# Kernel optimization log

Hardware: AMD Instinct MI355X
Metric: run time of the kernel (lower is better)

## Reference

```python
import jax, jax.numpy as jnp
import numpy as np

NPOINT = 2048
NSAMPLE = 16
LEAKY = 0.1
BN_EPS = 1e-5


def square_distance(src, dst):
    # src [B,S,3], dst [B,N,3] -> [B,S,N] squared euclidean
    d = -2.0 * jnp.einsum('bsc,bnc->bsn', src, dst)
    d = d + jnp.sum(src * src, -1)[:, :, None]
    d = d + jnp.sum(dst * dst, -1)[:, None, :]
    return d


def furthest_point_sample(xyz, npoint):
    # xyz [B,N,3] -> idx [B,npoint]; matches pointnet2 CUDA (seed = index 0)
    B, N, _ = xyz.shape

    def step(carry, _):
        dist, far = carry  # dist [B,N], far [B]
        centroid = jnp.take_along_axis(xyz, far[:, None, None], axis=1)  # [B,1,3]
        d = jnp.sum((xyz - centroid) ** 2, axis=-1)
        dist = jnp.minimum(dist, d)
        nxt = jnp.argmax(dist, axis=-1).astype(jnp.int32)
        return (dist, nxt), far

    init = (jnp.full((B, N), 1e10, xyz.dtype), jnp.zeros((B,), jnp.int32))
    _, idxs = jax.lax.scan(step, init, None, length=npoint)
    return idxs.T  # [B, npoint]


def _gather_nbrs(p, i):
    # p [N,C], i [S,K] -> [S,K,C]
    return p[i]


gather_group = jax.vmap(_gather_nbrs)


def conv_bn_lrelu(x, W, g, b):
    # x [B,Cin,S,K], W [Cout,Cin]; 1x1 conv + train-mode BatchNorm2d + LeakyReLU
    y = jnp.einsum('oc,bcsk->bosk', W, x)
    mean = jnp.mean(y, axis=(0, 2, 3), keepdims=True)
    var = jnp.var(y, axis=(0, 2, 3), keepdims=True)
    y = (y - mean) * jax.lax.rsqrt(var + BN_EPS)
    y = y * g[None, :, None, None] + b[None, :, None, None]
    return jnp.where(y > 0, y, LEAKY * y)


def setup_inputs() -> dict:
    key = jax.random.key(0)
    ks = jax.random.split(key, 5)
    B, N, D = 4, 8192, 64
    return {
        'xyz': jax.random.normal(ks[0], (B, 3, N), jnp.float32),
        'points': jax.random.normal(ks[1], (B, D, N), jnp.float32),
        'conv0_w': jax.random.normal(ks[2], (64, 67), jnp.float32) * 0.05,
        'conv1_w': jax.random.normal(ks[3], (64, 64), jnp.float32) * 0.05,
        'conv2_w': jax.random.normal(ks[4], (128, 64), jnp.float32) * 0.05,
        'bn0_g': jnp.ones((64,), jnp.float32),
        'bn0_b': jnp.zeros((64,), jnp.float32),
        'bn1_g': jnp.ones((64,), jnp.float32),
        'bn1_b': jnp.zeros((64,), jnp.float32),
        'bn2_g': jnp.ones((128,), jnp.float32),
        'bn2_b': jnp.zeros((128,), jnp.float32),
    }


def reference(xyz, points, conv0_w, conv1_w, conv2_w,
              bn0_g, bn0_b, bn1_g, bn1_b, bn2_g, bn2_b):
    xyz_t = jnp.transpose(xyz, (0, 2, 1))      # [B,N,3]
    pts_t = jnp.transpose(points, (0, 2, 1))   # [B,N,D]

    fps_idx = furthest_point_sample(xyz_t, NPOINT)                       # [B,S]
    new_xyz = jnp.take_along_axis(xyz_t, fps_idx[:, :, None], axis=1)    # [B,S,3]

    sqrd = square_distance(new_xyz, xyz_t)                               # [B,S,N]
    _, idx = jax.lax.top_k(-sqrd, NSAMPLE)                               # [B,S,K]

    grouped_xyz = gather_group(xyz_t, idx)                               # [B,S,K,3]
    grouped_norm = grouped_xyz - new_xyz[:, :, None, :]
    grouped_pts = gather_group(pts_t, idx)                               # [B,S,K,D]
    new_points = jnp.concatenate([grouped_norm, grouped_pts], axis=-1)   # [B,S,K,D+3]
    new_points = jnp.transpose(new_points, (0, 3, 1, 2))                 # [B,D+3,S,K]

    for W, g, b in ((conv0_w, bn0_g, bn0_b), (conv1_w, bn1_g, bn1_b),
                    (conv2_w, bn2_g, bn2_b)):
        new_points = conv_bn_lrelu(new_points, W, g, b)

    feat = jnp.max(new_points, axis=-1)                                  # [B,128,S]
    return jnp.transpose(new_xyz, (0, 2, 1)), feat, fps_idx
```

## Files before the change

### kernel.cpp

```cpp
#include <hip/hip_runtime.h>
#include <hip/hip_bf16.h>

#define BB 4
#define NP 8192
#define SS 2048
#define KK 16
#define DD 64
#define NN (BB*SS*KK)

__global__ __launch_bounds__(512) void fps_kernel(
    const float* __restrict__ xyz, float* __restrict__ newXyz,
    float* __restrict__ out)
{
  const int b = blockIdx.x;
  const int t = threadIdx.x;
  const int wv = t >> 6, l = t & 63;
  const float* xb = xyz + (size_t)b * 3 * NP;

  __shared__ float lx[NP], ly[NP], lz[NP];
  __shared__ int   wis[SS];
  __shared__ unsigned long long swin[2][8];

  float px[16], py[16], pz[16], dist[16];
#pragma unroll
  for (int j = 0; j < 16; j++) {
    int i = t + (j << 9);
    float x = xb[i], y = xb[NP + i], z = xb[2 * NP + i];
    px[j] = x; py[j] = y; pz[j] = z; dist[j] = 1e10f;
    lx[i] = x; ly[i] = y; lz[i] = z;
  }
  if (t == 0) wis[0] = 0;
  __syncthreads();

  int ii = 0;
  for (int it = 1; it < SS; ++it) {
    float cx = lx[ii], cy = ly[ii], cz = lz[ii];
    float best = -1.0f; int bi = 0;
#pragma unroll
    for (int j = 0; j < 16; j++) {
      float dx = __fsub_rn(px[j], cx);
      float dy = __fsub_rn(py[j], cy);
      float dz = __fsub_rn(pz[j], cz);
      float d = __fadd_rn(__fadd_rn(__fmul_rn(dx, dx), __fmul_rn(dy, dy)), __fmul_rn(dz, dz));
      float dm = fminf(dist[j], d);
      dist[j] = dm;
      if (dm > best) { best = dm; bi = t + (j << 9); }
    }
    unsigned long long pk =
        ((unsigned long long)__float_as_uint(best) << 32) | (unsigned)(~bi);
#pragma unroll
    for (int m = 1; m < 64; m <<= 1) {
      unsigned long long o = __shfl_xor(pk, m, 64);
      pk = (o > pk) ? o : pk;
    }
    int p = it & 1;
    if (l == 0) swin[p][wv] = pk;
    __syncthreads();
    unsigned long long v = swin[p][l & 7];
#pragma unroll
    for (int m = 1; m < 8; m <<= 1) {
      unsigned long long o = __shfl_xor(v, m, 64);
      v = (o > v) ? o : v;
    }
    ii = (int)(~((unsigned)v));
    if (t == 0) wis[it] = ii;
  }
  __syncthreads();

  float* outX = out;
  float* outI = out + 24576 + 1048576;
  for (int s = t; s < SS; s += 512) {
    int iw = wis[s];
    float x = lx[iw], y = ly[iw], z = lz[iw];
    size_t q = (size_t)(b * SS + s);
    newXyz[q * 3 + 0] = x;
    newXyz[q * 3 + 1] = y;
    newXyz[q * 3 + 2] = z;
    outX[(b * 3 + 0) * SS + s] = x;
    outX[(b * 3 + 1) * SS + s] = y;
    outX[(b * 3 + 2) * SS + s] = z;
    outI[b * SS + s] = (float)iw;
  }
}

__global__ __launch_bounds__(256) void knn_kernel(
    const float* __restrict__ xyz, const float* __restrict__ newXyz,
    int* __restrict__ knnIdx)
{
  const int t = threadIdx.x, w = t >> 6, l = t & 63;
  const int q = blockIdx.x * 4 + w;
  const int b = q >> 11;
  const float* xb = xyz + (size_t)b * 3 * NP;
  float qx = newXyz[q * 3], qy = newXyz[q * 3 + 1], qz = newXyz[q * 3 + 2];
  float ss = __fadd_rn(__fadd_rn(__fmul_rn(qx, qx), __fmul_rn(qy, qy)), __fmul_rn(qz, qz));
  float kd[16]; int ki[16];
#pragma unroll
  for (int j = 0; j < 16; j++) { kd[j] = __builtin_inff(); ki[j] = 0x7fffffff; }

  for (int m = 0; m < 128; m++) {
    int i = l + (m << 6);
    float x = xb[i], y = xb[NP + i], z = xb[2 * NP + i];
    float dot = __fadd_rn(__fadd_rn(__fmul_rn(x, qx), __fmul_rn(y, qy)), __fmul_rn(z, qz));
    float nn  = __fadd_rn(__fadd_rn(__fmul_rn(x, x), __fmul_rn(y, y)), __fmul_rn(z, z));
    float d   = __fadd_rn(__fadd_rn(__fmul_rn(-2.0f, dot), ss), nn);
    if (d < kd[15]) {
      kd[15] = d; ki[15] = i;
#pragma unroll
      for (int jj = 15; jj >= 1; jj--) {
        if (kd[jj] < kd[jj - 1]) {
          float td = kd[jj]; kd[jj] = kd[jj - 1]; kd[jj - 1] = td;
          int   ti = ki[jj]; ki[jj] = ki[jj - 1]; ki[jj - 1] = ti;
        }
      }
    }
  }

  __shared__ float sd[4 * 64 * 17];
  __shared__ int   sx[4 * 64 * 17];
  int base = (w * 64 + l) * 17;
#pragma unroll
  for (int j = 0; j < 16; j++) { sd[base + j] = kd[j]; sx[base + j] = ki[j]; }
  __syncthreads();

  int cur = 0; int outIdx = 0;
#pragma unroll 1
  for (int r = 0; r < 16; r++) {
    float hv = (cur < 16) ? sd[base + cur] : __builtin_inff();
    int   hi = (cur < 16) ? sx[base + cur] : 0x7fffffff;
    int   hl = l;
#pragma unroll
    for (int m2 = 1; m2 < 64; m2 <<= 1) {
      float ov = __shfl_xor(hv, m2, 64);
      int   oi = __shfl_xor(hi, m2, 64);
      int   ol = __shfl_xor(hl, m2, 64);
      if (ov < hv || (ov == hv && oi < hi)) { hv = ov; hi = oi; hl = ol; }
    }
    if (l == hl) cur++;
    if (l == r) outIdx = hi;
  }
  if (l < 16) knnIdx[q * 16 + l] = outIdx;
}

__global__ __launch_bounds__(256) void build_x0(
    const float* __restrict__ xyz, const float* __restrict__ points,
    const float* __restrict__ newXyz, const int* __restrict__ knnIdx,
    float* __restrict__ X)
{
  int n = blockIdx.x * 256 + threadIdx.x;
  int b = n >> 15;
  int q = n >> 4;
  int ip = knnIdx[n];
  const float* xb = xyz + (size_t)b * 3 * NP;
  X[(size_t)0 * NN + n] = xb[ip]          - newXyz[q * 3 + 0];
  X[(size_t)1 * NN + n] = xb[NP + ip]     - newXyz[q * 3 + 1];
  X[(size_t)2 * NN + n] = xb[2 * NP + ip] - newXyz[q * 3 + 2];
  const float* pb = points + (size_t)b * DD * NP;
#pragma unroll 8
  for (int d0 = 0; d0 < DD; d0++)
    X[(size_t)(3 + d0) * NN + n] = pb[(size_t)d0 * NP + ip];
}

template <int CIN, int COUT>
__global__ __launch_bounds__(256) void conv_kernel(
    const float* __restrict__ X, const float* __restrict__ W, float* __restrict__ Y)
{
  int n = blockIdx.x * 256 + threadIdx.x;
  float x[CIN];
#pragma unroll
  for (int c = 0; c < CIN; c++) x[c] = X[(size_t)c * NN + n];
#pragma unroll 1
  for (int o = 0; o < COUT; o += 4) {
    float a0 = 0.f, a1 = 0.f, a2 = 0.f, a3 = 0.f;
#pragma unroll
    for (int c = 0; c < CIN; c++) {
      float xv = x[c];
      a0 = fmaf(W[(o + 0) * CIN + c], xv, a0);
      a1 = fmaf(W[(o + 1) * CIN + c], xv, a1);
      a2 = fmaf(W[(o + 2) * CIN + c], xv, a2);
      a3 = fmaf(W[(o + 3) * CIN + c], xv, a3);
    }
    Y[(size_t)(o + 0) * NN + n] = a0;
    Y[(size_t)(o + 1) * NN + n] = a1;
    Y[(size_t)(o + 2) * NN + n] = a2;
    Y[(size_t)(o + 3) * NN + n] = a3;
  }
}

__global__ __launch_bounds__(256) void stats_kernel(
    const float* __restrict__ Y, float* __restrict__ stats)
{
  int c = blockIdx.y;
  int base = blockIdx.x * 4096 + threadIdx.x;
  const float* yc = Y + (size_t)c * NN;
  float s1 = 0.f, s2 = 0.f;
#pragma unroll
  for (int j = 0; j < 16; j++) {
    float v = yc[base + j * 256];
    s1 += v; s2 = fmaf(v, v, s2);
  }
#pragma unroll
  for (int m = 1; m < 64; m <<= 1) {
    s1 += __shfl_xor(s1, m, 64);
    s2 += __shfl_xor(s2, m, 64);
  }
  __shared__ float r1[4], r2[4];
  int w = threadIdx.x >> 6;
  if ((threadIdx.x & 63) == 0) { r1[w] = s1; r2[w] = s2; }
  __syncthreads();
  if (threadIdx.x == 0) {
    float t1 = r1[0] + r1[1] + r1[2] + r1[3];
    float t2 = r2[0] + r2[1] + r2[2] + r2[3];
    atomicAdd(&stats[c * 2], t1);
    atomicAdd(&stats[c * 2 + 1], t2);
  }
}

__global__ __launch_bounds__(256) void bn_lrelu_kernel(
    float* __restrict__ Y, const float* __restrict__ stats,
    const float* __restrict__ g, const float* __restrict__ bt)
{
  int c = blockIdx.y;
  int n = blockIdx.x * 256 + threadIdx.x;
  float mean = stats[c * 2] * (1.0f / NN);
  float var  = stats[c * 2 + 1] * (1.0f / NN) - mean * mean;
  float inv  = rsqrtf(var + 1e-5f);
  float gamma = g[c], beta = bt[c];
  size_t o = (size_t)c * NN + n;
  float v = (Y[o] - mean) * inv;
  v = v * gamma + beta;
  Y[o] = v > 0.0f ? v : 0.1f * v;
}

__global__ __launch_bounds__(256) void maxk_kernel(
    const float* __restrict__ X, float* __restrict__ out)
{
  int m = blockIdx.x * 256 + threadIdx.x;
  int s = m & 2047;
  int o = (m >> 11) & 127;
  int b = m >> 18;
  const float4* p = (const float4*)(X + (size_t)o * NN + ((size_t)((b << 11) + s) << 4));
  float4 v0 = p[0], v1 = p[1], v2 = p[2], v3 = p[3];
  float mx = fmaxf(fmaxf(fmaxf(v0.x, v0.y), fmaxf(v0.z, v0.w)),
                   fmaxf(fmaxf(v1.x, v1.y), fmaxf(v1.z, v1.w)));
  mx = fmaxf(mx, fmaxf(fmaxf(fmaxf(v2.x, v2.y), fmaxf(v2.z, v2.w)),
                       fmaxf(fmaxf(v3.x, v3.y), fmaxf(v3.z, v3.w))));
  out[24576 + (size_t)((b << 7) + o) * SS + s] = mx;
}

extern "C" void kernel_launch(void* const* d_in, const int* in_sizes, int n_in,
                              void* d_out, int out_size, void* d_ws, size_t ws_size,
                              hipStream_t stream) {
  const float* xyz    = (const float*)d_in[0];
  const float* points = (const float*)d_in[1];
  const float* w0 = (const float*)d_in[2];
  const float* w1 = (const float*)d_in[3];
  const float* w2 = (const float*)d_in[4];
  const float* g0 = (const float*)d_in[5];
  const float* b0 = (const float*)d_in[6];
  const float* g1 = (const float*)d_in[7];
  const float* b1 = (const float*)d_in[8];
  const float* g2 = (const float*)d_in[9];
  const float* b2 = (const float*)d_in[10];
  float* out = (float*)d_out;

  float* wsf    = (float*)d_ws;
  float* newXyz = wsf;
  int*   knnIdx = (int*)(wsf + 24576);
  float* stats  = wsf + 155648;
  float* Xa     = wsf + 155904;
  float* Xb     = wsf + 8937728;

  fps_kernel<<<BB, 512, 0, stream>>>(xyz, newXyz, out);
  knn_kernel<<<SS * BB / 4, 256, 0, stream>>>(xyz, newXyz, knnIdx);
  build_x0<<<NN / 256, 256, 0, stream>>>(xyz, points, newXyz, knnIdx, Xa);

  hipMemsetAsync(stats, 0, 256 * 4, stream);
  conv_kernel<67, 64><<<NN / 256, 256, 0, stream>>>(Xa, w0, Xb);
  stats_kernel<<<dim3(32, 64), 256, 0, stream>>>(Xb, stats);
  bn_lrelu_kernel<<<dim3(NN / 256, 64), 256, 0, stream>>>(Xb, stats, g0, b0);

  hipMemsetAsync(stats, 0, 256 * 4, stream);
  conv_kernel<64, 64><<<NN / 256, 256, 0, stream>>>(Xb, w1, Xa);
  stats_kernel<<<dim3(32, 64), 256, 0, stream>>>(Xa, stats);
  bn_lrelu_kernel<<<dim3(NN / 256, 64), 256, 0, stream>>>(Xa, stats, g1, b1);

  hipMemsetAsync(stats, 0, 256 * 4, stream);
  conv_kernel<64, 128><<<NN / 256, 256, 0, stream>>>(Xa, w2, Xb);
  stats_kernel<<<dim3(32, 128), 256, 0, stream>>>(Xb, stats);
  bn_lrelu_kernel<<<dim3(NN / 256, 128), 256, 0, stream>>>(Xb, stats, g2, b2);

  maxk_kernel<<<(BB * 128 * SS) / 256, 256, 0, stream>>>(Xb, out);
}
```

Measured before the change: 2.769 ms.

## Use DPP float max reduction and LDS atomicMax in FPS argmax

The per-iteration argmax in furthest point sampling now reduces a plain float max across each wave using DPP/swizzle lane ops instead of six 64-bit shuffle steps on packed value/index pairs. Only lanes holding the wave maximum recover their index and publish a packed key to shared memory with atomicMax. Three rotating slots let a single barrier per iteration suffice instead of a barrier plus a second cross-wave shuffle reduction. This shortens the serial critical path of the 2047-iteration loop, at the cost of LDS atomic contention and a rescan of the dist registers in the winning lanes.

```diff
diff --git a/kernel.cpp b/kernel.cpp
--- a/kernel.cpp
+++ b/kernel.cpp
@@ -8,18 +8,33 @@
 #define DD 64
 #define NN (BB*SS*KK)
 
+__device__ __forceinline__ float wave_max_f32(float v) {
+  int x;
+  x = __builtin_amdgcn_update_dpp(0, __float_as_int(v), 0xB1, 0xF, 0xF, true);
+  v = fmaxf(v, __int_as_float(x));
+  x = __builtin_amdgcn_update_dpp(0, __float_as_int(v), 0x4E, 0xF, 0xF, true);
+  v = fmaxf(v, __int_as_float(x));
+  x = __builtin_amdgcn_update_dpp(0, __float_as_int(v), 0x141, 0xF, 0xF, true);
+  v = fmaxf(v, __int_as_float(x));
+  x = __builtin_amdgcn_update_dpp(0, __float_as_int(v), 0x140, 0xF, 0xF, true);
+  v = fmaxf(v, __int_as_float(x));
+  x = __builtin_amdgcn_ds_swizzle(__float_as_int(v), 0x401F);
+  v = fmaxf(v, __int_as_float(x));
+  v = fmaxf(v, __shfl_xor(v, 32, 64));
+  return v;
+}
+
 __global__ __launch_bounds__(512) void fps_kernel(
     const float* __restrict__ xyz, float* __restrict__ newXyz,
     float* __restrict__ out)
 {
   const int b = blockIdx.x;
   const int t = threadIdx.x;
-  const int wv = t >> 6, l = t & 63;
   const float* xb = xyz + (size_t)b * 3 * NP;
 
   __shared__ float lx[NP], ly[NP], lz[NP];
   __shared__ int   wis[SS];
-  __shared__ unsigned long long swin[2][8];
+  __shared__ unsigned long long swin[3];
 
   float px[16], py[16], pz[16], dist[16];
 #pragma unroll
@@ -29,13 +44,13 @@
     px[j] = x; py[j] = y; pz[j] = z; dist[j] = 1e10f;
     lx[i] = x; ly[i] = y; lz[i] = z;
   }
-  if (t == 0) wis[0] = 0;
+  if (t == 0) { wis[0] = 0; swin[0] = 0; swin[1] = 0; swin[2] = 0; }
   __syncthreads();
 
-  int ii = 0;
+  float cx = lx[0], cy = ly[0], cz = lz[0];
+
   for (int it = 1; it < SS; ++it) {
-    float cx = lx[ii], cy = ly[ii], cz = lz[ii];
-    float best = -1.0f; int bi = 0;
+    float lbest = -1.0f;
 #pragma unroll
     for (int j = 0; j < 16; j++) {
       float dx = __fsub_rn(px[j], cx);
@@ -44,26 +59,25 @@
       float d = __fadd_rn(__fadd_rn(__fmul_rn(dx, dx), __fmul_rn(dy, dy)), __fmul_rn(dz, dz));
       float dm = fminf(dist[j], d);
       dist[j] = dm;
-      if (dm > best) { best = dm; bi = t + (j << 9); }
-    }
-    unsigned long long pk =
-        ((unsigned long long)__float_as_uint(best) << 32) | (unsigned)(~bi);
-#pragma unroll
-    for (int m = 1; m < 64; m <<= 1) {
-      unsigned long long o = __shfl_xor(pk, m, 64);
-      pk = (o > pk) ? o : pk;
-    }
-    int p = it & 1;
-    if (l == 0) swin[p][wv] = pk;
+      lbest = fmaxf(lbest, dm);
+    }
+    float Vw = wave_max_f32(lbest);
+    int q = it % 3;
+    if (lbest == Vw) {
+      unsigned mi = 0u;
+#pragma unroll
+      for (int j = 15; j >= 0; j--) {
+        if (dist[j] == Vw) mi = (unsigned)(t + (j << 9));
+      }
+      unsigned long long pk =
+          ((unsigned long long)__float_as_uint(Vw) << 32) | (unsigned)(~mi);
+      atomicMax(&swin[q], pk);
+    }
     __syncthreads();
-    unsigned long long v = swin[p][l & 7];
-#pragma unroll
-    for (int m = 1; m < 8; m <<= 1) {
-      unsigned long long o = __shfl_xor(v, m, 64);
-      v = (o > v) ? o : v;
-    }
-    ii = (int)(~((unsigned)v));
-    if (t == 0) wis[it] = ii;
+    unsigned long long pkf = swin[q];
+    int ii = (int)(~((unsigned)pkf));
+    if (t == 0) { wis[it] = ii; swin[(q + 2) % 3] = 0; }
+    cx = lx[ii]; cy = ly[ii]; cz = lz[ii];
   }
   __syncthreads();
 
@@ -72,10 +86,10 @@
   for (int s = t; s < SS; s += 512) {
     int iw = wis[s];
     float x = lx[iw], y = ly[iw], z = lz[iw];
-    size_t q = (size_t)(b * SS + s);
-    newXyz[q * 3 + 0] = x;
-    newXyz[q * 3 + 1] = y;
-    newXyz[q * 3 + 2] = z;
+    size_t qq = (size_t)(b * SS + s);
+    newXyz[qq * 3 + 0] = x;
+    newXyz[qq * 3 + 1] = y;
+    newXyz[qq * 3 + 2] = z;
     outX[(b * 3 + 0) * SS + s] = x;
     outX[(b * 3 + 1) * SS + s] = y;
     outX[(b * 3 + 2) * SS + s] = z;
```

Measured after the change: 2.735 ms. Within noise of the previous version (-1.2%).
